# Optimization experiments

Measured on AMD Instinct MI355X. Metric: run time of the kernel, lower is better.

## Reference

```python
import jax, jax.numpy as jnp
import numpy as np

N, C, T, H, W = 256, 512, 4, 8, 8
NUM_CLIPS = 8


def conv3(x, w):
    # x: [N,C,T,H,W], w: [O,I,1,3,3], padding (0,1,1) as in HR2O_NL
    return jax.lax.conv_general_dilated(
        x, w, window_strides=(1, 1, 1),
        padding=((0, 0), (1, 1), (1, 1)),
        dimension_numbers=('NCDHW', 'OIDHW', 'NCDHW'))


def setup_inputs() -> dict:
    key = jax.random.key(0)
    ks = jax.random.split(key, 8)
    w_scale = 1.0 / np.sqrt(C * 9)
    return {
        'x': jax.random.normal(ks[0], (N, C, T, H, W), dtype=jnp.float32),
        'roi_inds': jax.random.randint(ks[1], (N,), 0, NUM_CLIPS, dtype=jnp.int32),
        'Wq': jax.random.normal(ks[2], (C, C, 1, 3, 3), dtype=jnp.float32) * w_scale,
        'Wk': jax.random.normal(ks[3], (C, C, 1, 3, 3), dtype=jnp.float32) * w_scale,
        'Wv': jax.random.normal(ks[4], (C, C, 1, 3, 3), dtype=jnp.float32) * w_scale,
        'Wc': jax.random.normal(ks[5], (C, C, 1, 3, 3), dtype=jnp.float32) * w_scale,
        'gn_gamma': jnp.ones((C,), dtype=jnp.float32),
        'gn_beta': jnp.zeros((C,), dtype=jnp.float32),
    }


def reference(x, roi_inds, Wq, Wk, Wv, Wc, gn_gamma, gn_beta):
    q = conv3(x, Wq)            # [N,C,T,H,W]
    k = conv3(x, Wk)
    v = conv3(x, Wv)
    scale = 1.0 / jnp.sqrt(jnp.asarray(C, x.dtype))
    # pairwise channel dot per spatiotemporal location: [N,N,T,H,W]
    att = jnp.einsum('icthw,jcthw->ijthw', q, k) * scale
    same_group = (roi_inds[:, None] == roi_inds[None, :])  # [N,N]
    att = jnp.where(same_group[:, :, None, None, None], att, -jnp.inf)
    att = jax.nn.softmax(att, axis=1)  # per-group softmax (diagonal always valid)
    virt = jnp.einsum('ijthw,jcthw->icthw', att, v)  # [N,C,T,H,W]
    # GroupNorm, num_groups=1 (normalize over C,T,H,W per sample), affine
    mu = virt.mean(axis=(1, 2, 3, 4), keepdims=True)
    var = virt.var(axis=(1, 2, 3, 4), keepdims=True)
    virt = (virt - mu) * jax.lax.rsqrt(var + 1e-5)
    virt = virt * gn_gamma[None, :, None, None, None] + gn_beta[None, :, None, None, None]
    virt = jax.nn.relu(virt)
    virt = conv3(virt, Wc)
    return x + virt
```

## Files before the change

### kernel.cpp

```cpp
#include <hip/hip_runtime.h>
#include <hip/hip_bf16.h>

#define NN 256
#define CCH 512
#define TT 4
#define SS 64
#define LL 256

typedef unsigned short u16;
typedef unsigned int u32;

typedef __bf16 bf16_t;
typedef bf16_t bf16x8 __attribute__((ext_vector_type(8)));
typedef float f32x16 __attribute__((ext_vector_type(16)));

__device__ __forceinline__ float bf2f(u32 h){
    return __uint_as_float(h << 16);
}
__device__ __forceinline__ u16 f2bf(float f){
    u32 u = __float_as_uint(f);
    u32 r = u + 0x7fffu + ((u >> 16) & 1u);
    return (u16)(r >> 16);
}
__device__ __forceinline__ bf16x8 ldg8(const u16* p){
    uint4 q = *(const uint4*)p;
    return __builtin_bit_cast(bf16x8, q);
}
__device__ __forceinline__ bf16x8 ldl8(const u16* p){
    uint2 a = *(const uint2*)p;
    uint2 b = *(const uint2*)(p + 4);
    uint4 q; q.x = a.x; q.y = a.y; q.z = b.x; q.w = b.y;
    return __builtin_bit_cast(bf16x8, q);
}

__global__ __launch_bounds__(256) void wt_kernel(
    const float* __restrict__ W, u16* __restrict__ Wt)
{
    const int e = blockIdx.x * 256 + threadIdx.x;
    const int cl  = e & 15;
    const int o   = (e >> 4) & 511;
    const int cg  = (e >> 13) & 31;
    const int tap = e >> 18;
    Wt[e] = f2bf(W[((size_t)o * CCH + cg * 16 + cl) * 9 + tap]);
}

__global__ __launch_bounds__(256, 2) void conv_mfma_kernel(
    const float* __restrict__ x, const u16* __restrict__ Wt, u16* __restrict__ outb)
{
    __shared__ u16 lds[4 * 100 * 36];
    const int tid = threadIdx.x;
    const int n  = blockIdx.x;
    const int ob = blockIdx.y * 128;
    const int lane = tid & 63;
    const int w  = tid >> 6;
    const int wm = w & 1, wn = w >> 1;
    const int h   = lane >> 5;
    const int col = lane & 31;
    const int r  = col >> 3, cc = col & 7;

    for (int i = tid; i < 7200; i += 256) ((u32*)lds)[i] = 0;

    f32x16 acc[2][4];
    #pragma unroll
    for (int m = 0; m < 2; ++m)
      #pragma unroll
      for (int j = 0; j < 4; ++j)
        #pragma unroll
        for (int e = 0; e < 16; ++e) acc[m][j][e] = 0.f;

    const int cp2 = tid >> 4;
    const int s4  = (tid & 15) << 2;

    int bbase[4];
    #pragma unroll
    for (int j = 0; j < 4; ++j){
        const int nt = wn * 4 + j;
        const int p = nt >> 1, sh = nt & 1;
        bbase[j] = (p * 100 + (sh * 4 + r) * 10 + cc) * 36 + h * 8;
    }
    const size_t abase = (size_t)(ob + wm * 64 + col) * 16 + h * 8;

    for (int ch = 0; ch < 16; ++ch){
        const int c0 = ch * 32;
        __syncthreads();
        #pragma unroll
        for (int p = 0; p < 4; ++p){
            const float* xr = x + (((size_t)n * CCH + c0 + 2 * cp2) * TT + p) * SS + s4;
            const float4 v0 = *(const float4*)xr;
            const float4 v1 = *(const float4*)(xr + 256);
            const float a0[4] = {v0.x, v0.y, v0.z, v0.w};
            const float a1[4] = {v1.x, v1.y, v1.z, v1.w};
            #pragma unroll
            for (int i = 0; i < 4; ++i){
                const int s = s4 + i;
                const int sp = ((s >> 3) + 1) * 10 + (s & 7) + 1;
                ((u32*)lds)[(p * 100 + sp) * 18 + cp2] =
                    (u32)f2bf(a0[i]) | ((u32)f2bf(a1[i]) << 16);
            }
        }
        __syncthreads();
        #pragma unroll
        for (int tap = 0; tap < 9; ++tap){
            const int tof = ((tap / 3) * 10 + (tap % 3)) * 36;
            #pragma unroll
            for (int ks = 0; ks < 2; ++ks){
                const size_t ai = (size_t)(tap * 32 + ch * 2 + ks) * 8192 + abase;
                const bf16x8 a0 = ldg8(Wt + ai);
                const bf16x8 a1 = ldg8(Wt + ai + 512);
                bf16x8 bfr[4];
                #pragma unroll
                for (int j = 0; j < 4; ++j)
                    bfr[j] = ldl8(&lds[bbase[j] + tof + ks * 16]);
                #pragma unroll
                for (int j = 0; j < 4; ++j){
                    acc[0][j] = __builtin_amdgcn_mfma_f32_32x32x16_bf16(a0, bfr[j], acc[0][j], 0, 0, 0);
                    acc[1][j] = __builtin_amdgcn_mfma_f32_32x32x16_bf16(a1, bfr[j], acc[1][j], 0, 0, 0);
                }
            }
        }
    }

    #pragma unroll
    for (int m = 0; m < 2; ++m){
        #pragma unroll
        for (int j = 0; j < 4; ++j){
            const int nt = wn * 4 + j;
            const int p = nt >> 1, sh = nt & 1;
            const int loc = p * SS + sh * 32 + col;
            u16* orow = outb + ((size_t)loc * NN + n) * CCH + ob + wm * 64 + m * 32;
            #pragma unroll
            for (int g2 = 0; g2 < 4; ++g2){
                uint2 val;
                val.x = (u32)f2bf(acc[m][j][g2 * 4 + 0]) | ((u32)f2bf(acc[m][j][g2 * 4 + 1]) << 16);
                val.y = (u32)f2bf(acc[m][j][g2 * 4 + 2]) | ((u32)f2bf(acc[m][j][g2 * 4 + 3]) << 16);
                *(uint2*)&orow[g2 * 8 + h * 4] = val;
            }
        }
    }
}

__global__ __launch_bounds__(256, 2) void conv_out_mfma_kernel(
    const u16* __restrict__ virtb, const u16* __restrict__ Wt,
    const float* __restrict__ x, const float* __restrict__ gamma,
    const float* __restrict__ beta, const float* __restrict__ musig,
    float* __restrict__ out)
{
    __shared__ u16 lds[4 * 100 * 36];
    const int tid = threadIdx.x;
    const int n  = blockIdx.x;
    const int ob = blockIdx.y * 128;
    const int lane = tid & 63;
    const int w  = tid >> 6;
    const int wm = w & 1, wn = w >> 1;
    const int h   = lane >> 5;
    const int col = lane & 31;
    const int r  = col >> 3, cc = col & 7;

    const float mu   = musig[2 * n];
    const float rsig = musig[2 * n + 1];

    for (int i = tid; i < 7200; i += 256) ((u32*)lds)[i] = 0;

    f32x16 acc[2][4];
    #pragma unroll
    for (int m = 0; m < 2; ++m)
      #pragma unroll
      for (int j = 0; j < 4; ++j)
        #pragma unroll
        for (int e = 0; e < 16; ++e) acc[m][j][e] = 0.f;

    const int cp = tid & 15;
    const int sg = tid >> 4;

    int bbase[4];
    #pragma unroll
    for (int j = 0; j < 4; ++j){
        const int nt = wn * 4 + j;
        const int p = nt >> 1, sh = nt & 1;
        bbase[j] = (p * 100 + (sh * 4 + r) * 10 + cc) * 36 + h * 8;
    }
    const size_t abase = (size_t)(ob + wm * 64 + col) * 16 + h * 8;

    for (int ch = 0; ch < 16; ++ch){
        const int c0 = ch * 32;
        const float g0 = gamma[c0 + 2 * cp], g1 = gamma[c0 + 2 * cp + 1];
        const float b0 = beta [c0 + 2 * cp], b1 = beta [c0 + 2 * cp + 1];
        __syncthreads();
        #pragma unroll
        for (int p = 0; p < 4; ++p){
            #pragma unroll
            for (int i = 0; i < 4; ++i){
                const int s = sg * 4 + i;
                const u32 wv = *(const u32*)(virtb + ((size_t)(p * SS + s) * NN + n) * CCH + c0 + 2 * cp);
                const float f0 = fmaxf((bf2f(wv & 0xffffu) - mu) * rsig * g0 + b0, 0.f);
                const float f1 = fmaxf((bf2f(wv >> 16)     - mu) * rsig * g1 + b1, 0.f);
                const int sp = ((s >> 3) + 1) * 10 + (s & 7) + 1;
                ((u32*)lds)[(p * 100 + sp) * 18 + cp] =
                    (u32)f2bf(f0) | ((u32)f2bf(f1) << 16);
            }
        }
        __syncthreads();
        #pragma unroll
        for (int tap = 0; tap < 9; ++tap){
            const int tof = ((tap / 3) * 10 + (tap % 3)) * 36;
            #pragma unroll
            for (int ks = 0; ks < 2; ++ks){
                const size_t ai = (size_t)(tap * 32 + ch * 2 + ks) * 8192 + abase;
                const bf16x8 a0 = ldg8(Wt + ai);
                const bf16x8 a1 = ldg8(Wt + ai + 512);
                bf16x8 bfr[4];
                #pragma unroll
                for (int j = 0; j < 4; ++j)
                    bfr[j] = ldl8(&lds[bbase[j] + tof + ks * 16]);
                #pragma unroll
                for (int j = 0; j < 4; ++j){
                    acc[0][j] = __builtin_amdgcn_mfma_f32_32x32x16_bf16(a0, bfr[j], acc[0][j], 0, 0, 0);
                    acc[1][j] = __builtin_amdgcn_mfma_f32_32x32x16_bf16(a1, bfr[j], acc[1][j], 0, 0, 0);
                }
            }
        }
    }

    #pragma unroll
    for (int m = 0; m < 2; ++m){
        #pragma unroll
        for (int j = 0; j < 4; ++j){
            const int nt = wn * 4 + j;
            const int p = nt >> 1, sh = nt & 1;
            const int s = sh * 32 + col;
            #pragma unroll
            for (int g2 = 0; g2 < 4; ++g2){
                const int o0 = ob + wm * 64 + m * 32 + 8 * g2 + 4 * h;
                #pragma unroll
                for (int rr = 0; rr < 4; ++rr){
                    const size_t oi = (((size_t)n * CCH + o0 + rr) * TT + p) * SS + s;
                    out[oi] = x[oi] + acc[m][j][g2 * 4 + rr];
                }
            }
        }
    }
}

__global__ __launch_bounds__(256) void vt_kernel(
    const u16* __restrict__ vb, u16* __restrict__ vt)
{
    __shared__ u16 ts[64][72];
    const int loc = blockIdx.x;
    const int n0 = (blockIdx.y & 3) * 64;
    const int c0 = (blockIdx.y >> 2) * 64;
    const int tid = threadIdx.x;
    const int rr = tid >> 3;
    const int ct = tid & 7;
    #pragma unroll
    for (int q = 0; q < 2; ++q){
        const int row = rr + q * 32;
        const int key = (row & 7) ^ ((row >> 3) & 7);
        const uint4 v = *(const uint4*)(vb + ((size_t)loc * NN + n0 + row) * CCH + c0 + ct * 8);
        *(uint4*)&ts[row][(ct ^ key) << 3] = v;
    }
    __syncthreads();
    #pragma unroll
    for (int q = 0; q < 2; ++q){
        const int c = rr + q * 32;
        u16 tmp[8];
        #pragma unroll
        for (int e = 0; e < 8; ++e){
            const int n = ct * 8 + e;
            const int key = (n & 7) ^ ((n >> 3) & 7);
            tmp[e] = ts[n][(((c >> 3) ^ key) << 3) + (c & 7)];
        }
        uint4 o;
        o.x = (u32)tmp[0] | ((u32)tmp[1] << 16);
        o.y = (u32)tmp[2] | ((u32)tmp[3] << 16);
        o.z = (u32)tmp[4] | ((u32)tmp[5] << 16);
        o.w = (u32)tmp[6] | ((u32)tmp[7] << 16);
        *(uint4*)(vt + ((size_t)loc * CCH + c0 + c) * NN + n0 + ct * 8) = o;
    }
}

__global__ __launch_bounds__(256, 3) void attn_mfma_kernel(
    const u16* __restrict__ qb, const u16* __restrict__ kb,
    const u16* __restrict__ vt, const int* __restrict__ roi,
    u16* __restrict__ virtb)
{
    __shared__ float Srow[32][264];
    __shared__ u16 Pfrag[16 * 64 * 8];
    __shared__ int roi_s[256];

    const int bid = blockIdx.x;
    const int loc = ((bid >> 6) << 3) | (bid & 7);
    const int it  = (bid >> 3) & 7;
    const int i0  = it * 32;
    const int tid = threadIdx.x;
    const int lane = tid & 63;
    const int w   = tid >> 6;
    const int h   = lane >> 5;
    const int col = lane & 31;

    roi_s[tid] = roi[tid];

    f32x16 acc0, acc1;
    #pragma unroll
    for (int e = 0; e < 16; ++e){ acc0[e] = 0.f; acc1[e] = 0.f; }

    const u16* qp = qb + ((size_t)loc * NN + i0 + col) * CCH + h * 8;
    const u16* kp = kb + ((size_t)loc * NN + w * 64 + col) * CCH + h * 8;

    #pragma unroll 4
    for (int kc = 0; kc < 32; ++kc){
        const bf16x8 a  = ldg8(qp + kc * 16);
        const bf16x8 b0 = ldg8(kp + kc * 16);
        const bf16x8 b1 = ldg8(kp + 32 * CCH + kc * 16);
        acc0 = __builtin_amdgcn_mfma_f32_32x32x16_bf16(a, b0, acc0, 0, 0, 0);
        acc1 = __builtin_amdgcn_mfma_f32_32x32x16_bf16(a, b1, acc1, 0, 0, 0);
    }

    #pragma unroll
    for (int e = 0; e < 16; ++e){
        const int r = (e & 3) + 8 * (e >> 2) + 4 * h;
        Srow[r][w * 64 + col]      = acc0[e];
        Srow[r][w * 64 + 32 + col] = acc1[e];
    }
    __syncthreads();

    {
        const int row = tid >> 3, u = tid & 7;
        const int myroi = roi_s[i0 + row];
        const float scale = 0.04419417382415922f;
        float ev[32];
        float mx = -1e30f;
        #pragma unroll
        for (int g = 0; g < 8; ++g){
            const float4 s4 = *(const float4*)&Srow[row][u * 4 + g * 32];
            const float ss[4] = {s4.x, s4.y, s4.z, s4.w};
            #pragma unroll
            for (int q = 0; q < 4; ++q){
                const int j = u * 4 + g * 32 + q;
                const float xv = (roi_s[j] == myroi) ? ss[q] * scale : -1e30f;
                ev[g * 4 + q] = xv;
                mx = fmaxf(mx, xv);
            }
        }
        mx = fmaxf(mx, __shfl_xor(mx, 1));
        mx = fmaxf(mx, __shfl_xor(mx, 2));
        mx = fmaxf(mx, __shfl_xor(mx, 4));
        float ssum = 0.f;
        #pragma unroll
        for (int q2 = 0; q2 < 32; ++q2){
            const float e2 = (ev[q2] > -1e29f) ? __expf(ev[q2] - mx) : 0.f;
            ev[q2] = e2;
            ssum += e2;
        }
// ... 27 lines not shown
        #pragma unroll
        for (int jn = 0; jn < 4; ++jn){
            const bf16x8 bv = ldg8(vp + (size_t)(jn * 32) * NN + t * 16);
            pacc[jn] = __builtin_amdgcn_mfma_f32_32x32x16_bf16(pa, bv, pacc[jn], 0, 0, 0);
        }
    }

    u16* op = virtb + ((size_t)loc * NN + i0) * CCH + w * 128 + col;
    #pragma unroll
    for (int jn = 0; jn < 4; ++jn){
        #pragma unroll
        for (int e = 0; e < 16; ++e){
            const int r = (e & 3) + 8 * (e >> 2) + 4 * h;
            op[(size_t)r * CCH + jn * 32] = f2bf(pacc[jn][e]);
        }
    }
}

__global__ __launch_bounds__(256) void stats_kernel(
    const u16* __restrict__ virtb, float* __restrict__ musig)
{
    const int n = blockIdx.x;
    const int tid = threadIdx.x;
    float s = 0.f, q = 0.f;
    for (int loc = 0; loc < LL; ++loc){
        const u32 v = *(const u32*)(virtb + ((size_t)loc * NN + n) * CCH + 2 * tid);
        const float a = bf2f(v & 0xffffu);
        const float b = bf2f(v >> 16);
        s += a + b;
        q += a * a + b * b;
    }
    #pragma unroll
    for (int off = 1; off < 64; off <<= 1){
        s += __shfl_xor(s, off);
        q += __shfl_xor(q, off);
    }
    __shared__ float red[8];
    const int wave = tid >> 6;
    if ((tid & 63) == 0){ red[wave * 2] = s; red[wave * 2 + 1] = q; }
    __syncthreads();
    if (tid == 0){
        const float S = red[0] + red[2] + red[4] + red[6];
        const float Q = red[1] + red[3] + red[5] + red[7];
        const float inv = 1.f / 131072.f;
        const float mval = S * inv;
        const float var = Q * inv - mval * mval;
        musig[2 * n]     = mval;
        musig[2 * n + 1] = rsqrtf(var + 1e-5f);
    }
}

__global__ void sentinel_kernel(float* out){
    const size_t i = (size_t)blockIdx.x * 256 + threadIdx.x;
    out[i] = 1.0e9f;
}

extern "C" void kernel_launch(void* const* d_in, const int* in_sizes, int n_in,
                              void* d_out, int out_size, void* d_ws, size_t ws_size,
                              hipStream_t stream)
{
    (void)in_sizes; (void)n_in; (void)out_size;
    const float* x   = (const float*)d_in[0];
    const int*   roi = (const int*)d_in[1];
    const float* Wq  = (const float*)d_in[2];
    const float* Wk  = (const float*)d_in[3];
    const float* Wv  = (const float*)d_in[4];
    const float* Wc  = (const float*)d_in[5];
    const float* gam = (const float*)d_in[6];
    const float* bet = (const float*)d_in[7];
    float* out = (float*)d_out;

    const size_t EL = 33554432ull;
    const size_t need = EL * 2ull * 4ull + 2048ull;
    if (ws_size < need){
        sentinel_kernel<<<131072, 256, 0, stream>>>(out);
        return;
    }
    u16* qb    = (u16*)d_ws;
    u16* kb    = qb + EL;
    u16* vb    = kb + EL;
    u16* virtb = vb + EL;
    float* musig = (float*)(virtb + EL);

    u16* WtA = (u16*)d_out;
    u16* vt  = (u16*)d_out + (1u << 22);
    u16* WtC = qb;

    const dim3 cgrid(256, 4);

    wt_kernel<<<9216, 256, 0, stream>>>(Wq, WtA);
    conv_mfma_kernel<<<cgrid, 256, 0, stream>>>(x, WtA, qb);
    wt_kernel<<<9216, 256, 0, stream>>>(Wk, WtA);
    conv_mfma_kernel<<<cgrid, 256, 0, stream>>>(x, WtA, kb);
    wt_kernel<<<9216, 256, 0, stream>>>(Wv, WtA);
    conv_mfma_kernel<<<cgrid, 256, 0, stream>>>(x, WtA, vb);

    vt_kernel<<<dim3(256, 32), 256, 0, stream>>>(vb, vt);
    attn_mfma_kernel<<<2048, 256, 0, stream>>>(qb, kb, vt, roi, virtb);
    stats_kernel<<<256, 256, 0, stream>>>(virtb, musig);

    wt_kernel<<<9216, 256, 0, stream>>>(Wc, WtC);
    conv_out_mfma_kernel<<<cgrid, 256, 0, stream>>>(virtb, WtC, x, gam, bet, musig, out);
}
```

Before: 1.734 ms.

## Give each wave a private double-buffered LDS tile and drop block barriers in convs

Both conv kernels now give each wave ownership of one time slice (p = wave index) with its own double-buffered LDS region. That removes the block-wide __syncthreads, and the next channel chunk's global loads overlap the current chunk's MFMAs. Each wave now computes 128 output channels by 64 spatial positions (4x2 tiles) instead of 64x128, which changes the A/B operand reuse mix. The LDS row stride is padded from 36 to 40 so B fragments load as single 16-byte reads, and input staging uses 16-byte stores. The costs are more LDS per block (64KB), more global A-fragment loads per wave, and more registers held by the prefetch buffers, which may hurt occupancy.

```diff
diff --git a/kernel.cpp b/kernel.cpp
--- a/kernel.cpp
+++ b/kernel.cpp
@@ -24,12 +24,6 @@
 }
 __device__ __forceinline__ bf16x8 ldg8(const u16* p){
     uint4 q = *(const uint4*)p;
-    return __builtin_bit_cast(bf16x8, q);
-}
-__device__ __forceinline__ bf16x8 ldl8(const u16* p){
-    uint2 a = *(const uint2*)p;
-    uint2 b = *(const uint2*)(p + 4);
-    uint4 q; q.x = a.x; q.y = a.y; q.z = b.x; q.w = b.y;
     return __builtin_bit_cast(bf16x8, q);
 }
 
@@ -47,92 +41,105 @@
 __global__ __launch_bounds__(256, 2) void conv_mfma_kernel(
     const float* __restrict__ x, const u16* __restrict__ Wt, u16* __restrict__ outb)
 {
-    __shared__ u16 lds[4 * 100 * 36];
+    __shared__ u16 lds[8 * 4000];
     const int tid = threadIdx.x;
     const int n  = blockIdx.x;
     const int ob = blockIdx.y * 128;
     const int lane = tid & 63;
     const int w  = tid >> 6;
-    const int wm = w & 1, wn = w >> 1;
     const int h   = lane >> 5;
     const int col = lane & 31;
     const int r  = col >> 3, cc = col & 7;
 
-    for (int i = tid; i < 7200; i += 256) ((u32*)lds)[i] = 0;
-
-    f32x16 acc[2][4];
-    #pragma unroll
-    for (int m = 0; m < 2; ++m)
+    {
+        u32* wb = (u32*)(lds + w * 8000);
+        for (int i = lane; i < 4000; i += 64) wb[i] = 0;
+    }
+
+    f32x16 acc[4][2];
+    #pragma unroll
+    for (int m = 0; m < 4; ++m)
       #pragma unroll
-      for (int j = 0; j < 4; ++j)
-        #pragma unroll
-        for (int e = 0; e < 16; ++e) acc[m][j][e] = 0.f;
-
-    const int cp2 = tid >> 4;
-    const int s4  = (tid & 15) << 2;
-
-    int bbase[4];
-    #pragma unroll
-    for (int j = 0; j < 4; ++j){
-        const int nt = wn * 4 + j;
-        const int p = nt >> 1, sh = nt & 1;
-        bbase[j] = (p * 100 + (sh * 4 + r) * 10 + cc) * 36 + h * 8;
-    }
-    const size_t abase = (size_t)(ob + wm * 64 + col) * 16 + h * 8;
+      for (int nt = 0; nt < 2; ++nt)
+        #pragma unroll
+        for (int e = 0; e < 16; ++e) acc[m][nt][e] = 0.f;
+
+    const int g  = lane >> 4;
+    const int s4 = (lane & 15) << 2;
+
+    int bbase[2];
+    #pragma unroll
+    for (int nt = 0; nt < 2; ++nt)
+        bbase[nt] = ((nt * 4 + r) * 10 + cc) * 40 + h * 8;
+
+    const size_t abase = (size_t)(ob + col) * 16 + h * 8;
+
+    auto stage_load = [&](int ch, float4* xv){
+        const float* xr = x + (((size_t)n * CCH + ch * 32 + g * 8) * TT + w) * SS + s4;
+        #pragma unroll
+        for (int c2 = 0; c2 < 8; ++c2)
+            xv[c2] = *(const float4*)(xr + (size_t)c2 * (TT * SS));
+    };
+    auto stage_write = [&](int ch, const float4* xv){
+        u16* wb = lds + w * 8000 + (ch & 1) * 4000;
+        #pragma unroll
+        for (int i = 0; i < 4; ++i){
+            const int s = s4 + i;
+            const int sp = ((s >> 3) + 1) * 10 + (s & 7) + 1;
+            uint4 pw;
+            pw.x = (u32)f2bf(((const float*)&xv[0])[i]) | ((u32)f2bf(((const float*)&xv[1])[i]) << 16);
+            pw.y = (u32)f2bf(((const float*)&xv[2])[i]) | ((u32)f2bf(((const float*)&xv[3])[i]) << 16);
+            pw.z = (u32)f2bf(((const float*)&xv[4])[i]) | ((u32)f2bf(((const float*)&xv[5])[i]) << 16);
+            pw.w = (u32)f2bf(((const float*)&xv[6])[i]) | ((u32)f2bf(((const float*)&xv[7])[i]) << 16);
+            *(uint4*)&wb[sp * 40 + g * 8] = pw;
+        }
+    };
+
+    {
+        float4 xv[8];
+        stage_load(0, xv);
+        stage_write(0, xv);
+    }
 
     for (int ch = 0; ch < 16; ++ch){
-        const int c0 = ch * 32;
-        __syncthreads();
-        #pragma unroll
-        for (int p = 0; p < 4; ++p){
-            const float* xr = x + (((size_t)n * CCH + c0 + 2 * cp2) * TT + p) * SS + s4;
-            const float4 v0 = *(const float4*)xr;
-            const float4 v1 = *(const float4*)(xr + 256);
-            const float a0[4] = {v0.x, v0.y, v0.z, v0.w};
-            const float a1[4] = {v1.x, v1.y, v1.z, v1.w};
-            #pragma unroll
-            for (int i = 0; i < 4; ++i){
-                const int s = s4 + i;
-                const int sp = ((s >> 3) + 1) * 10 + (s & 7) + 1;
-                ((u32*)lds)[(p * 100 + sp) * 18 + cp2] =
-                    (u32)f2bf(a0[i]) | ((u32)f2bf(a1[i]) << 16);
-            }
-        }
-        __syncthreads();
+        float4 xv[8];
+        if (ch < 15) stage_load(ch + 1, xv);
+
+        const u16* wb = lds + w * 8000 + (ch & 1) * 4000;
         #pragma unroll
         for (int tap = 0; tap < 9; ++tap){
-            const int tof = ((tap / 3) * 10 + (tap % 3)) * 36;
+            const int tof = ((tap / 3) * 10 + (tap % 3)) * 40;
             #pragma unroll
             for (int ks = 0; ks < 2; ++ks){
                 const size_t ai = (size_t)(tap * 32 + ch * 2 + ks) * 8192 + abase;
-                const bf16x8 a0 = ldg8(Wt + ai);
-                const bf16x8 a1 = ldg8(Wt + ai + 512);
-                bf16x8 bfr[4];
-                #pragma unroll
-                for (int j = 0; j < 4; ++j)
-                    bfr[j] = ldl8(&lds[bbase[j] + tof + ks * 16]);
-                #pragma unroll
-                for (int j = 0; j < 4; ++j){
-                    acc[0][j] = __builtin_amdgcn_mfma_f32_32x32x16_bf16(a0, bfr[j], acc[0][j], 0, 0, 0);
-                    acc[1][j] = __builtin_amdgcn_mfma_f32_32x32x16_bf16(a1, bfr[j], acc[1][j], 0, 0, 0);
-                }
+                bf16x8 a[4];
+                #pragma unroll
+                for (int m = 0; m < 4; ++m) a[m] = ldg8(Wt + ai + 512 * m);
+                bf16x8 b[2];
+                #pragma unroll
+                for (int nt = 0; nt < 2; ++nt)
+                    b[nt] = ldg8(&wb[bbase[nt] + tof + ks * 16]);
+                #pragma unroll
+                for (int m = 0; m < 4; ++m)
+                  #pragma unroll
+                  for (int nt = 0; nt < 2; ++nt)
+                    acc[m][nt] = __builtin_amdgcn_mfma_f32_32x32x16_bf16(a[m], b[nt], acc[m][nt], 0, 0, 0);
             }
         }
-    }
-
-    #pragma unroll
-    for (int m = 0; m < 2; ++m){
-        #pragma unroll
-        for (int j = 0; j < 4; ++j){
-            const int nt = wn * 4 + j;
-            const int p = nt >> 1, sh = nt & 1;
-            const int loc = p * SS + sh * 32 + col;
-            u16* orow = outb + ((size_t)loc * NN + n) * CCH + ob + wm * 64 + m * 32;
+        if (ch < 15) stage_write(ch + 1, xv);
+    }
+
+    #pragma unroll
+    for (int m = 0; m < 4; ++m){
+        #pragma unroll
+        for (int nt = 0; nt < 2; ++nt){
+            const int loc = w * 64 + nt * 32 + col;
+            u16* orow = outb + ((size_t)loc * NN + n) * CCH + ob + m * 32;
             #pragma unroll
             for (int g2 = 0; g2 < 4; ++g2){
                 uint2 val;
-                val.x = (u32)f2bf(acc[m][j][g2 * 4 + 0]) | ((u32)f2bf(acc[m][j][g2 * 4 + 1]) << 16);
-                val.y = (u32)f2bf(acc[m][j][g2 * 4 + 2]) | ((u32)f2bf(acc[m][j][g2 * 4 + 3]) << 16);
+                val.x = (u32)f2bf(acc[m][nt][g2 * 4 + 0]) | ((u32)f2bf(acc[m][nt][g2 * 4 + 1]) << 16);
+                val.y = (u32)f2bf(acc[m][nt][g2 * 4 + 2]) | ((u32)f2bf(acc[m][nt][g2 * 4 + 3]) << 16);
                 *(uint2*)&orow[g2 * 8 + h * 4] = val;
             }
         }
@@ -145,13 +152,12 @@
     const float* __restrict__ beta, const float* __restrict__ musig,
     float* __restrict__ out)
 {
-    __shared__ u16 lds[4 * 100 * 36];
+    __shared__ u16 lds[8 * 4000];
     const int tid = threadIdx.x;
     const int n  = blockIdx.x;
     const int ob = blockIdx.y * 128;
     const int lane = tid & 63;
     const int w  = tid >> 6;
-    const int wm = w & 1, wn = w >> 1;
     const int h   = lane >> 5;
     const int col = lane & 31;
     const int r  = col >> 3, cc = col & 7;
@@ -159,82 +165,117 @@
     const float mu   = musig[2 * n];
     const float rsig = musig[2 * n + 1];
 
-    for (int i = tid; i < 7200; i += 256) ((u32*)lds)[i] = 0;
-
-    f32x16 acc[2][4];
-    #pragma unroll
-    for (int m = 0; m < 2; ++m)
+    {
+        u32* wb = (u32*)(lds + w * 8000);
+        for (int i = lane; i < 4000; i += 64) wb[i] = 0;
+    }
+
+    f32x16 acc[4][2];
+    #pragma unroll
+    for (int m = 0; m < 4; ++m)
       #pragma unroll
-      for (int j = 0; j < 4; ++j)
-        #pragma unroll
-        for (int e = 0; e < 16; ++e) acc[m][j][e] = 0.f;
-
-    const int cp = tid & 15;
-    const int sg = tid >> 4;
-
-    int bbase[4];
-    #pragma unroll
-    for (int j = 0; j < 4; ++j){
-        const int nt = wn * 4 + j;
-        const int p = nt >> 1, sh = nt & 1;
-        bbase[j] = (p * 100 + (sh * 4 + r) * 10 + cc) * 36 + h * 8;
-    }
-    const size_t abase = (size_t)(ob + wm * 64 + col) * 16 + h * 8;
+      for (int nt = 0; nt < 2; ++nt)
+        #pragma unroll
+        for (int e = 0; e < 16; ++e) acc[m][nt][e] = 0.f;
+
+    const int g  = lane >> 4;
+    const int s4 = (lane & 15) << 2;
+
+    int bbase[2];
+    #pragma unroll
+    for (int nt = 0; nt < 2; ++nt)
+        bbase[nt] = ((nt * 4 + r) * 10 + cc) * 40 + h * 8;
+
+    const size_t abase = (size_t)(ob + col) * 16 + h * 8;
+
+    auto stage_load = [&](int ch, uint4* vv){
+        #pragma unroll
+        for (int i = 0; i < 4; ++i)
+            vv[i] = *(const uint4*)(virtb + ((size_t)(w * 64 + s4 + i) * NN + n) * CCH + ch * 32 + g * 8);
+    };
+    auto stage_write = [&](int ch, const uint4* vv){
+        const float* gp = gamma + ch * 32 + g * 8;
+        const float* bp = beta  + ch * 32 + g * 8;
+        const float4 ga0 = *(const float4*)gp;
+        const float4 ga1 = *(const float4*)(gp + 4);
+        const float4 be0 = *(const float4*)bp;
+        const float4 be1 = *(const float4*)(bp + 4);
+        float gsc[8], off[8];
+        const float gav[8] = {ga0.x, ga0.y, ga0.z, ga0.w, ga1.x, ga1.y, ga1.z, ga1.w};
+        const float bev[8] = {be0.x, be0.y, be0.z, be0.w, be1.x, be1.y, be1.z, be1.w};
+        #pragma unroll
+        for (int c2 = 0; c2 < 8; ++c2){
+            gsc[c2] = gav[c2] * rsig;
+            off[c2] = bev[c2] - mu * rsig * gav[c2];
+        }
+        u16* wb = lds + w * 8000 + (ch & 1) * 4000;
+        #pragma unroll
+        for (int i = 0; i < 4; ++i){
+            const int s = s4 + i;
+            const int sp = ((s >> 3) + 1) * 10 + (s & 7) + 1;
+            const u32 q[4] = {vv[i].x, vv[i].y, vv[i].z, vv[i].w};
+            u16 ov[8];
+            #pragma unroll
+            for (int c2 = 0; c2 < 8; ++c2){
+                const u32 half = (c2 & 1) ? (q[c2 >> 1] >> 16) : (q[c2 >> 1] & 0xffffu);
+                const float f = fmaxf(bf2f(half) * gsc[c2] + off[c2], 0.f);
+                ov[c2] = f2bf(f);
+            }
+            uint4 pw;
+            pw.x = (u32)ov[0] | ((u32)ov[1] << 16);
+            pw.y = (u32)ov[2] | ((u32)ov[3] << 16);
+            pw.z = (u32)ov[4] | ((u32)ov[5] << 16);
+            pw.w = (u32)ov[6] | ((u32)ov[7] << 16);
+            *(uint4*)&wb[sp * 40 + g * 8] = pw;
+        }
+    };
+
+    {
+        uint4 vv[4];
+        stage_load(0, vv);
+        stage_write(0, vv);
+    }
 
     for (int ch = 0; ch < 16; ++ch){
-        const int c0 = ch * 32;
-        const float g0 = gamma[c0 + 2 * cp], g1 = gamma[c0 + 2 * cp + 1];
-        const float b0 = beta [c0 + 2 * cp], b1 = beta [c0 + 2 * cp + 1];
-        __syncthreads();
-        #pragma unroll
-        for (int p = 0; p < 4; ++p){
-            #pragma unroll
-            for (int i = 0; i < 4; ++i){
-                const int s = sg * 4 + i;
-                const u32 wv = *(const u32*)(virtb + ((size_t)(p * SS + s) * NN + n) * CCH + c0 + 2 * cp);
-                const float f0 = fmaxf((bf2f(wv & 0xffffu) - mu) * rsig * g0 + b0, 0.f);
-                const float f1 = fmaxf((bf2f(wv >> 16)     - mu) * rsig * g1 + b1, 0.f);
-                const int sp = ((s >> 3) + 1) * 10 + (s & 7) + 1;
-                ((u32*)lds)[(p * 100 + sp) * 18 + cp] =
-                    (u32)f2bf(f0) | ((u32)f2bf(f1) << 16);
-            }
-        }
-        __syncthreads();
+        uint4 vv[4];
+        if (ch < 15) stage_load(ch + 1, vv);
+
+        const u16* wb = lds + w * 8000 + (ch & 1) * 4000;
         #pragma unroll
         for (int tap = 0; tap < 9; ++tap){
-            const int tof = ((tap / 3) * 10 + (tap % 3)) * 36;
+            const int tof = ((tap / 3) * 10 + (tap % 3)) * 40;
             #pragma unroll
             for (int ks = 0; ks < 2; ++ks){
                 const size_t ai = (size_t)(tap * 32 + ch * 2 + ks) * 8192 + abase;
-                const bf16x8 a0 = ldg8(Wt + ai);
-                const bf16x8 a1 = ldg8(Wt + ai + 512);
-                bf16x8 bfr[4];
-                #pragma unroll
-                for (int j = 0; j < 4; ++j)
-                    bfr[j] = ldl8(&lds[bbase[j] + tof + ks * 16]);
-                #pragma unroll
-                for (int j = 0; j < 4; ++j){
-                    acc[0][j] = __builtin_amdgcn_mfma_f32_32x32x16_bf16(a0, bfr[j], acc[0][j], 0, 0, 0);
-                    acc[1][j] = __builtin_amdgcn_mfma_f32_32x32x16_bf16(a1, bfr[j], acc[1][j], 0, 0, 0);
-                }
+                bf16x8 a[4];
+                #pragma unroll
+                for (int m = 0; m < 4; ++m) a[m] = ldg8(Wt + ai + 512 * m);
+                bf16x8 b[2];
+                #pragma unroll
+                for (int nt = 0; nt < 2; ++nt)
+                    b[nt] = ldg8(&wb[bbase[nt] + tof + ks * 16]);
+                #pragma unroll
+                for (int m = 0; m < 4; ++m)
+                  #pragma unroll
+                  for (int nt = 0; nt < 2; ++nt)
+                    acc[m][nt] = __builtin_amdgcn_mfma_f32_32x32x16_bf16(a[m], b[nt], acc[m][nt], 0, 0, 0);
             }
         }
-    }
-
-    #pragma unroll
-    for (int m = 0; m < 2; ++m){
-        #pragma unroll
-        for (int j = 0; j < 4; ++j){
-            const int nt = wn * 4 + j;
-            const int p = nt >> 1, sh = nt & 1;
-            const int s = sh * 32 + col;
+        if (ch < 15) stage_write(ch + 1, vv);
+    }
+
+    #pragma unroll
+    for (int m = 0; m < 4; ++m){
+        #pragma unroll
+        for (int nt = 0; nt < 2; ++nt){
+            const int s = nt * 32 + col;
             #pragma unroll
             for (int g2 = 0; g2 < 4; ++g2){
-                const int o0 = ob + wm * 64 + m * 32 + 8 * g2 + 4 * h;
+                const int o0 = ob + m * 32 + 8 * g2 + 4 * h;
                 #pragma unroll
                 for (int rr = 0; rr < 4; ++rr){
-                    const size_t oi = (((size_t)n * CCH + o0 + rr) * TT + p) * SS + s;
-                    out[oi] = x[oi] + acc[m][j][g2 * 4 + rr];
+                    const size_t oi = (((size_t)n * CCH + o0 + rr) * TT + w) * SS + s;
+                    out[oi] = x[oi] + acc[m][nt][g2 * 4 + rr];
                 }
             }
         }
```

Result: slower. 2.108 ms (+21.5%).

## Double-buffer LDS input tiles and prefetch next channel chunk in both convs

Applied to the files above, without the earlier changes.

Both implicit-GEMM conv kernels now use two LDS buffers. The next 32-channel chunk is loaded from global memory into registers before the MFMA loop over the current chunk, then written into the other buffer afterwards, leaving one barrier per iteration instead of two. The LDS row stride goes from 36 to 40 halves so the B-fragment reads become single 16-byte loads, and the staging writes become 16-byte stores with a per-wave layout. In the output conv, the GroupNorm affine is folded into a scale and offset. The cost is LDS growing to about 64KB per block and extra registers for the prefetch, which could limit the two-blocks-per-CU occupancy.

```diff
diff --git a/kernel.cpp b/kernel.cpp
--- a/kernel.cpp
+++ b/kernel.cpp
@@ -24,12 +24,6 @@
 }
 __device__ __forceinline__ bf16x8 ldg8(const u16* p){
     uint4 q = *(const uint4*)p;
-    return __builtin_bit_cast(bf16x8, q);
-}
-__device__ __forceinline__ bf16x8 ldl8(const u16* p){
-    uint2 a = *(const uint2*)p;
-    uint2 b = *(const uint2*)(p + 4);
-    uint4 q; q.x = a.x; q.y = a.y; q.z = b.x; q.w = b.y;
     return __builtin_bit_cast(bf16x8, q);
 }
 
@@ -47,7 +41,7 @@
 __global__ __launch_bounds__(256, 2) void conv_mfma_kernel(
     const float* __restrict__ x, const u16* __restrict__ Wt, u16* __restrict__ outb)
 {
-    __shared__ u16 lds[4 * 100 * 36];
+    __shared__ u16 lds[2 * 4 * 100 * 40];
     const int tid = threadIdx.x;
     const int n  = blockIdx.x;
     const int ob = blockIdx.y * 128;
@@ -58,7 +52,7 @@
     const int col = lane & 31;
     const int r  = col >> 3, cc = col & 7;
 
-    for (int i = tid; i < 7200; i += 256) ((u32*)lds)[i] = 0;
+    for (int i = tid; i < 16000; i += 256) ((u32*)lds)[i] = 0;
 
     f32x16 acc[2][4];
     #pragma unroll
@@ -68,40 +62,55 @@
         #pragma unroll
         for (int e = 0; e < 16; ++e) acc[m][j][e] = 0.f;
 
-    const int cp2 = tid >> 4;
-    const int s4  = (tid & 15) << 2;
+    const int g  = lane >> 4;
+    const int sl = lane & 15;
 
     int bbase[4];
     #pragma unroll
     for (int j = 0; j < 4; ++j){
         const int nt = wn * 4 + j;
         const int p = nt >> 1, sh = nt & 1;
-        bbase[j] = (p * 100 + (sh * 4 + r) * 10 + cc) * 36 + h * 8;
+        bbase[j] = (p * 100 + (sh * 4 + r) * 10 + cc) * 40 + h * 8;
     }
     const size_t abase = (size_t)(ob + wm * 64 + col) * 16 + h * 8;
 
+    auto stage_load = [&](int ch, float4* xv){
+        const float* xr = x + (((size_t)n * CCH + ch * 32 + g * 8) * TT + w) * SS + sl * 4;
+        #pragma unroll
+        for (int c2 = 0; c2 < 8; ++c2)
+            xv[c2] = *(const float4*)(xr + (size_t)c2 * (TT * SS));
+    };
+    auto stage_write = [&](int buf, const float4* xv){
+        u16* wb = lds + buf * 16000 + w * 4000;
+        #pragma unroll
+        for (int i = 0; i < 4; ++i){
+            const int s = sl * 4 + i;
+            const int sp = ((s >> 3) + 1) * 10 + (s & 7) + 1;
+            uint4 pw;
+            pw.x = (u32)f2bf(((const float*)&xv[0])[i]) | ((u32)f2bf(((const float*)&xv[1])[i]) << 16);
+            pw.y = (u32)f2bf(((const float*)&xv[2])[i]) | ((u32)f2bf(((const float*)&xv[3])[i]) << 16);
+            pw.z = (u32)f2bf(((const float*)&xv[4])[i]) | ((u32)f2bf(((const float*)&xv[5])[i]) << 16);
+            pw.w = (u32)f2bf(((const float*)&xv[6])[i]) | ((u32)f2bf(((const float*)&xv[7])[i]) << 16);
+            *(uint4*)&wb[sp * 40 + g * 8] = pw;
+        }
+    };
+
+    {
+        float4 xv[8];
+        stage_load(0, xv);
+        __syncthreads();
+        stage_write(0, xv);
+    }
+    __syncthreads();
+
     for (int ch = 0; ch < 16; ++ch){
-        const int c0 = ch * 32;
-        __syncthreads();
-        #pragma unroll
-        for (int p = 0; p < 4; ++p){
-            const float* xr = x + (((size_t)n * CCH + c0 + 2 * cp2) * TT + p) * SS + s4;
-            const float4 v0 = *(const float4*)xr;
-            const float4 v1 = *(const float4*)(xr + 256);
-            const float a0[4] = {v0.x, v0.y, v0.z, v0.w};
-            const float a1[4] = {v1.x, v1.y, v1.z, v1.w};
-            #pragma unroll
-            for (int i = 0; i < 4; ++i){
-                const int s = s4 + i;
-                const int sp = ((s >> 3) + 1) * 10 + (s & 7) + 1;
-                ((u32*)lds)[(p * 100 + sp) * 18 + cp2] =
-                    (u32)f2bf(a0[i]) | ((u32)f2bf(a1[i]) << 16);
-            }
-        }
-        __syncthreads();
+        float4 xv[8];
+        if (ch < 15) stage_load(ch + 1, xv);
+
+        const u16* cb = lds + (ch & 1) * 16000;
         #pragma unroll
         for (int tap = 0; tap < 9; ++tap){
-            const int tof = ((tap / 3) * 10 + (tap % 3)) * 36;
+            const int tof = ((tap / 3) * 10 + (tap % 3)) * 40;
             #pragma unroll
             for (int ks = 0; ks < 2; ++ks){
                 const size_t ai = (size_t)(tap * 32 + ch * 2 + ks) * 8192 + abase;
@@ -110,7 +119,7 @@
                 bf16x8 bfr[4];
                 #pragma unroll
                 for (int j = 0; j < 4; ++j)
-                    bfr[j] = ldl8(&lds[bbase[j] + tof + ks * 16]);
+                    bfr[j] = ldg8(&cb[bbase[j] + tof + ks * 16]);
                 #pragma unroll
                 for (int j = 0; j < 4; ++j){
                     acc[0][j] = __builtin_amdgcn_mfma_f32_32x32x16_bf16(a0, bfr[j], acc[0][j], 0, 0, 0);
@@ -118,6 +127,8 @@
                 }
             }
         }
+        if (ch < 15) stage_write((ch + 1) & 1, xv);
+        __syncthreads();
     }
 
     #pragma unroll
@@ -145,7 +156,7 @@
     const float* __restrict__ beta, const float* __restrict__ musig,
     float* __restrict__ out)
 {
-    __shared__ u16 lds[4 * 100 * 36];
+    __shared__ u16 lds[2 * 4 * 100 * 40];
     const int tid = threadIdx.x;
     const int n  = blockIdx.x;
     const int ob = blockIdx.y * 128;
@@ -159,7 +170,7 @@
     const float mu   = musig[2 * n];
     const float rsig = musig[2 * n + 1];
 
-    for (int i = tid; i < 7200; i += 256) ((u32*)lds)[i] = 0;
+    for (int i = tid; i < 16000; i += 256) ((u32*)lds)[i] = 0;
 
     f32x16 acc[2][4];
     #pragma unroll
@@ -169,40 +180,78 @@
         #pragma unroll
         for (int e = 0; e < 16; ++e) acc[m][j][e] = 0.f;
 
-    const int cp = tid & 15;
-    const int sg = tid >> 4;
+    const int g  = lane >> 4;
+    const int sl = lane & 15;
 
     int bbase[4];
     #pragma unroll
     for (int j = 0; j < 4; ++j){
         const int nt = wn * 4 + j;
         const int p = nt >> 1, sh = nt & 1;
-        bbase[j] = (p * 100 + (sh * 4 + r) * 10 + cc) * 36 + h * 8;
+        bbase[j] = (p * 100 + (sh * 4 + r) * 10 + cc) * 40 + h * 8;
     }
     const size_t abase = (size_t)(ob + wm * 64 + col) * 16 + h * 8;
 
+    auto stage_load = [&](int ch, uint4* vv){
+        #pragma unroll
+        for (int i = 0; i < 4; ++i){
+            const int s = sl * 4 + i;
+            vv[i] = *(const uint4*)(virtb + ((size_t)(w * SS + s) * NN + n) * CCH + ch * 32 + g * 8);
+        }
+    };
+    auto stage_write = [&](int ch, int buf, const uint4* vv){
+        const float* gp = gamma + ch * 32 + g * 8;
+        const float* bp = beta  + ch * 32 + g * 8;
+        const float4 ga0 = *(const float4*)gp;
+        const float4 ga1 = *(const float4*)(gp + 4);
+        const float4 be0 = *(const float4*)bp;
+        const float4 be1 = *(const float4*)(bp + 4);
+        const float gav[8] = {ga0.x, ga0.y, ga0.z, ga0.w, ga1.x, ga1.y, ga1.z, ga1.w};
+        const float bev[8] = {be0.x, be0.y, be0.z, be0.w, be1.x, be1.y, be1.z, be1.w};
+        float gsc[8], off[8];
+        #pragma unroll
+        for (int c2 = 0; c2 < 8; ++c2){
+            gsc[c2] = gav[c2] * rsig;
+            off[c2] = bev[c2] - mu * rsig * gav[c2];
+        }
+        u16* wb = lds + buf * 16000 + w * 4000;
+        #pragma unroll
+        for (int i = 0; i < 4; ++i){
+            const int s = sl * 4 + i;
+            const int sp = ((s >> 3) + 1) * 10 + (s & 7) + 1;
+            const u32 q[4] = {vv[i].x, vv[i].y, vv[i].z, vv[i].w};
+            u16 ov[8];
+            #pragma unroll
+            for (int c2 = 0; c2 < 8; ++c2){
+                const u32 half = (c2 & 1) ? (q[c2 >> 1] >> 16) : (q[c2 >> 1] & 0xffffu);
+                const float f = fmaxf(bf2f(half) * gsc[c2] + off[c2], 0.f);
+                ov[c2] = f2bf(f);
+            }
+            uint4 pw;
+            pw.x = (u32)ov[0] | ((u32)ov[1] << 16);
+            pw.y = (u32)ov[2] | ((u32)ov[3] << 16);
+            pw.z = (u32)ov[4] | ((u32)ov[5] << 16);
+            pw.w = (u32)ov[6] | ((u32)ov[7] << 16);
+            *(uint4*)&wb[sp * 40 + g * 8] = pw;
+        }
+    };
+
+    {
+        uint4 vv[4];
+        stage_load(0, vv);
+        __syncthreads();
+        stage_write(0, 0, vv);
+    }
+    __syncthreads();
+
     for (int ch = 0; ch < 16; ++ch){
-        const int c0 = ch * 32;
-        const float g0 = gamma[c0 + 2 * cp], g1 = gamma[c0 + 2 * cp + 1];
-        const float b0 = beta [c0 + 2 * cp], b1 = beta [c0 + 2 * cp + 1];
-        __syncthreads();
-        #pragma unroll
-        for (int p = 0; p < 4; ++p){
-            #pragma unroll
-            for (int i = 0; i < 4; ++i){
-                const int s = sg * 4 + i;
-                const u32 wv = *(const u32*)(virtb + ((size_t)(p * SS + s) * NN + n) * CCH + c0 + 2 * cp);
-                const float f0 = fmaxf((bf2f(wv & 0xffffu) - mu) * rsig * g0 + b0, 0.f);
-                const float f1 = fmaxf((bf2f(wv >> 16)     - mu) * rsig * g1 + b1, 0.f);
-                const int sp = ((s >> 3) + 1) * 10 + (s & 7) + 1;
-                ((u32*)lds)[(p * 100 + sp) * 18 + cp] =
-                    (u32)f2bf(f0) | ((u32)f2bf(f1) << 16);
-            }
-        }
-        __syncthreads();
+        uint4 vv[4];
+        if (ch < 15) stage_load(ch + 1, vv);
+
+        const u16* cb = lds + (ch & 1) * 16000;
         #pragma unroll
         for (int tap = 0; tap < 9; ++tap){
-            const int tof = ((tap / 3) * 10 + (tap % 3)) * 36;
+            const int tof = ((tap / 3) * 10 + (tap % 3)) * 40;
             #pragma unroll
             for (int ks = 0; ks < 2; ++ks){
                 const size_t ai = (size_t)(tap * 32 + ch * 2 + ks) * 8192 + abase;
@@ -211,7 +260,7 @@
                 bf16x8 bfr[4];
                 #pragma unroll
                 for (int j = 0; j < 4; ++j)
-                    bfr[j] = ldl8(&lds[bbase[j] + tof + ks * 16]);
+                    bfr[j] = ldg8(&cb[bbase[j] + tof + ks * 16]);
                 #pragma unroll
                 for (int j = 0; j < 4; ++j){
                     acc[0][j] = __builtin_amdgcn_mfma_f32_32x32x16_bf16(a0, bfr[j], acc[0][j], 0, 0, 0);
@@ -219,6 +268,8 @@
                 }
             }
         }
+        if (ch < 15) stage_write(ch + 1, (ch + 1) & 1, vv);
+        __syncthreads();
     }
 
     #pragma unroll
```

Result: faster. 1.697 ms (-2.1%).

## Pre-pad bf16 conv inputs and double-buffer them into LDS via direct global-to-LDS loads

Applied to the files above, without the earlier changes.

Adds separate kernels that convert x, and the normalized virt (GroupNorm+ReLU folded in), into padded, XOR-swizzled bf16 tiles in global memory. The conv kernels then stream each 32-channel chunk straight into LDS with global_load_lds, double-buffered so the next chunk loads during the current MFMA work, and read 16-byte swizzled fragments from LDS. This removes per-block f32-to-bf16 conversion, LDS zeroing and one barrier per chunk. The block index is also remapped over a 1D grid. It costs two extra passes over memory and workspace reuse (xpad shares space with vt, virtn uses kb), which depends on the kernel ordering staying correct.

```diff
diff --git a/kernel.cpp b/kernel.cpp
--- a/kernel.cpp
+++ b/kernel.cpp
@@ -26,11 +26,10 @@
     uint4 q = *(const uint4*)p;
     return __builtin_bit_cast(bf16x8, q);
 }
-__device__ __forceinline__ bf16x8 ldl8(const u16* p){
-    uint2 a = *(const uint2*)p;
-    uint2 b = *(const uint2*)(p + 4);
-    uint4 q; q.x = a.x; q.y = a.y; q.z = b.x; q.w = b.y;
-    return __builtin_bit_cast(bf16x8, q);
+__device__ __forceinline__ void gload_lds16(const u16* g, u16* l){
+    __builtin_amdgcn_global_load_lds(
+        (const __attribute__((address_space(1))) void*)g,
+        (__attribute__((address_space(3))) void*)l, 16, 0, 0);
 }
 
 __global__ __launch_bounds__(256) void wt_kernel(
@@ -44,13 +43,121 @@
     Wt[e] = f2bf(W[((size_t)o * CCH + cg * 16 + cl) * 9 + tap]);
 }
 
+__global__ __launch_bounds__(256) void xpad_kernel(
+    const float* __restrict__ x, u16* __restrict__ xpad)
+{
+    const int n  = blockIdx.x;
+    const int ch = blockIdx.y;
+    const int tid = threadIdx.x;
+    const int p  = tid >> 6;
+    const int cb = (tid >> 4) & 3;
+    const int s4 = (tid & 15) << 2;
+    u16* tile = xpad + ((size_t)n * 16 + ch) * 12800;
+
+    const float* xr = x + (((size_t)n * CCH + ch * 32 + cb * 8) * TT + p) * SS + s4;
+    float4 v[8];
+    #pragma unroll
+    for (int c2 = 0; c2 < 8; ++c2)
+        v[c2] = *(const float4*)(xr + (size_t)c2 * (TT * SS));
+    #pragma unroll
+    for (int i = 0; i < 4; ++i){
+        const int s = s4 + i;
+        const int sp = ((s >> 3) + 1) * 10 + (s & 7) + 1;
+        const int q = cb ^ (sp & 3);
+        uint4 pw;
+        pw.x = (u32)f2bf(((const float*)&v[0])[i]) | ((u32)f2bf(((const float*)&v[1])[i]) << 16);
+        pw.y = (u32)f2bf(((const float*)&v[2])[i]) | ((u32)f2bf(((const float*)&v[3])[i]) << 16);
+        pw.z = (u32)f2bf(((const float*)&v[4])[i]) | ((u32)f2bf(((const float*)&v[5])[i]) << 16);
+        pw.w = (u32)f2bf(((const float*)&v[6])[i]) | ((u32)f2bf(((const float*)&v[7])[i]) << 16);
+        *(uint4*)&tile[p * 3200 + sp * 32 + q * 8] = pw;
+    }
+    for (int bt = tid; bt < 576; bt += 256){
+        const int pp   = bt / 144;
+        const int bb   = bt % 144;
+        const int bi   = bb >> 2;
+        const int slot = bb & 3;
+        int sp;
+        if (bi < 10)      sp = bi;
+        else if (bi < 20) sp = 90 + (bi - 10);
+        else { const int k = (bi - 20) >> 1; sp = (k + 1) * 10 + ((bi - 20) & 1) * 9; }
+        uint4 z; z.x = 0; z.y = 0; z.z = 0; z.w = 0;
+        *(uint4*)&tile[pp * 3200 + sp * 32 + slot * 8] = z;
+    }
+}
+
+__global__ __launch_bounds__(256) void virtn_kernel(
+    const u16* __restrict__ virtb, const float* __restrict__ musig,
+    const float* __restrict__ gamma, const float* __restrict__ beta,
+    u16* __restrict__ vn)
+{
+    const int n  = blockIdx.x;
+    const int ch = blockIdx.y;
+    const int tid = threadIdx.x;
+    const int p  = tid >> 6;
+    const int cb = (tid >> 4) & 3;
+    const int s4 = (tid & 15) << 2;
+    u16* tile = vn + ((size_t)n * 16 + ch) * 12800;
+
+    const float mu   = musig[2 * n];
+    const float rsig = musig[2 * n + 1];
+    const int c0 = ch * 32 + cb * 8;
+    const float4 ga0 = *(const float4*)(gamma + c0);
+    const float4 ga1 = *(const float4*)(gamma + c0 + 4);
+    const float4 be0 = *(const float4*)(beta + c0);
+    const float4 be1 = *(const float4*)(beta + c0 + 4);
+    const float gav[8] = {ga0.x, ga0.y, ga0.z, ga0.w, ga1.x, ga1.y, ga1.z, ga1.w};
+    const float bev[8] = {be0.x, be0.y, be0.z, be0.w, be1.x, be1.y, be1.z, be1.w};
+    float gsc[8], off[8];
+    #pragma unroll
+    for (int c2 = 0; c2 < 8; ++c2){
+        gsc[c2] = gav[c2] * rsig;
+        off[c2] = bev[c2] - mu * rsig * gav[c2];
+    }
+
+    #pragma unroll
+    for (int i = 0; i < 4; ++i){
+        const int s = s4 + i;
+        const int loc = p * SS + s;
+        const uint4 wv = *(const uint4*)(virtb + ((size_t)loc * NN + n) * CCH + c0);
+        const u32 q4[4] = {wv.x, wv.y, wv.z, wv.w};
+        u16 ov[8];
+        #pragma unroll
+        for (int c2 = 0; c2 < 8; ++c2){
+            const u32 half = (c2 & 1) ? (q4[c2 >> 1] >> 16) : (q4[c2 >> 1] & 0xffffu);
+            ov[c2] = f2bf(fmaxf(bf2f(half) * gsc[c2] + off[c2], 0.f));
+        }
+        const int sp = ((s >> 3) + 1) * 10 + (s & 7) + 1;
+        const int q = cb ^ (sp & 3);
+        uint4 pw;
+        pw.x = (u32)ov[0] | ((u32)ov[1] << 16);
+        pw.y = (u32)ov[2] | ((u32)ov[3] << 16);
+        pw.z = (u32)ov[4] | ((u32)ov[5] << 16);
+        pw.w = (u32)ov[6] | ((u32)ov[7] << 16);
+        *(uint4*)&tile[p * 3200 + sp * 32 + q * 8] = pw;
+    }
+    for (int bt = tid; bt < 576; bt += 256){
+        const int pp   = bt / 144;
+        const int bb   = bt % 144;
+        const int bi   = bb >> 2;
+        const int slot = bb & 3;
+        int sp;
+        if (bi < 10)      sp = bi;
+        else if (bi < 20) sp = 90 + (bi - 10);
+        else { const int k = (bi - 20) >> 1; sp = (k + 1) * 10 + ((bi - 20) & 1) * 9; }
+        uint4 z; z.x = 0; z.y = 0; z.z = 0; z.w = 0;
+        *(uint4*)&tile[pp * 3200 + sp * 32 + slot * 8] = z;
+    }
+}
+
 __global__ __launch_bounds__(256, 2) void conv_mfma_kernel(
-    const float* __restrict__ x, const u16* __restrict__ Wt, u16* __restrict__ outb)
-{
-    __shared__ u16 lds[4 * 100 * 36];
-    const int tid = threadIdx.x;
-    const int n  = blockIdx.x;
-    const int ob = blockIdx.y * 128;
+    const u16* __restrict__ xp, const u16* __restrict__ Wt, u16* __restrict__ outb)
+{
+    __shared__ u16 lds[2 * 12800];
+    const int bid = blockIdx.x;
+    const int wk  = (bid & 7) * 128 + (bid >> 3);
+    const int n  = wk >> 2;
+    const int ob = (wk & 3) * 128;
+    const int tid = threadIdx.x;
     const int lane = tid & 63;
     const int w  = tid >> 6;
     const int wm = w & 1, wn = w >> 1;
@@ -58,8 +165,6 @@
     const int col = lane & 31;
     const int r  = col >> 3, cc = col & 7;
 
-    for (int i = tid; i < 7200; i += 256) ((u32*)lds)[i] = 0;
-
     f32x16 acc[2][4];
     #pragma unroll
     for (int m = 0; m < 2; ++m)
@@ -68,40 +173,31 @@
         #pragma unroll
         for (int e = 0; e < 16; ++e) acc[m][j][e] = 0.f;
 
-    const int cp2 = tid >> 4;
-    const int s4  = (tid & 15) << 2;
-
-    int bbase[4];
+    int pb[4], sp0[4];
     #pragma unroll
     for (int j = 0; j < 4; ++j){
         const int nt = wn * 4 + j;
-        const int p = nt >> 1, sh = nt & 1;
-        bbase[j] = (p * 100 + (sh * 4 + r) * 10 + cc) * 36 + h * 8;
+        pb[j]  = (nt >> 1) * 3200;
+        sp0[j] = ((nt & 1) * 4 + r) * 10 + cc;
     }
     const size_t abase = (size_t)(ob + wm * 64 + col) * 16 + h * 8;
+    const u16* srcn = xp + (size_t)n * (16 * 12800) + lane * 8;
+
+    auto stage = [&](int ch, int buf){
+        const u16* g = srcn + (size_t)ch * 12800;
+        for (int i = w; i < 25; i += 4)
+            gload_lds16(g + i * 512, &lds[buf * 12800 + i * 512]);
+    };
+
+    stage(0, 0);
+    __syncthreads();
 
     for (int ch = 0; ch < 16; ++ch){
-        const int c0 = ch * 32;
-        __syncthreads();
-        #pragma unroll
-        for (int p = 0; p < 4; ++p){
-            const float* xr = x + (((size_t)n * CCH + c0 + 2 * cp2) * TT + p) * SS + s4;
-            const float4 v0 = *(const float4*)xr;
-            const float4 v1 = *(const float4*)(xr + 256);
-            const float a0[4] = {v0.x, v0.y, v0.z, v0.w};
-            const float a1[4] = {v1.x, v1.y, v1.z, v1.w};
-            #pragma unroll
-            for (int i = 0; i < 4; ++i){
-                const int s = s4 + i;
-                const int sp = ((s >> 3) + 1) * 10 + (s & 7) + 1;
-                ((u32*)lds)[(p * 100 + sp) * 18 + cp2] =
-                    (u32)f2bf(a0[i]) | ((u32)f2bf(a1[i]) << 16);
-            }
-        }
-        __syncthreads();
+        if (ch < 15) stage(ch + 1, (ch + 1) & 1);
+        const u16* cbuf = &lds[(ch & 1) * 12800];
         #pragma unroll
         for (int tap = 0; tap < 9; ++tap){
-            const int tof = ((tap / 3) * 10 + (tap % 3)) * 36;
+            const int T = (tap / 3) * 10 + (tap % 3);
             #pragma unroll
             for (int ks = 0; ks < 2; ++ks){
                 const size_t ai = (size_t)(tap * 32 + ch * 2 + ks) * 8192 + abase;
@@ -109,8 +205,11 @@
                 const bf16x8 a1 = ldg8(Wt + ai + 512);
                 bf16x8 bfr[4];
                 #pragma unroll
-                for (int j = 0; j < 4; ++j)
-                    bfr[j] = ldl8(&lds[bbase[j] + tof + ks * 16]);
+                for (int j = 0; j < 4; ++j){
+                    const int sp = sp0[j] + T;
+                    const int idx = pb[j] + sp * 32 + ((((ks << 1) | h) ^ (sp & 3)) << 3);
+                    bfr[j] = ldg8(&cbuf[idx]);
+                }
                 #pragma unroll
                 for (int j = 0; j < 4; ++j){
                     acc[0][j] = __builtin_amdgcn_mfma_f32_32x32x16_bf16(a0, bfr[j], acc[0][j], 0, 0, 0);
@@ -118,6 +217,7 @@
                 }
             }
         }
+        __syncthreads();
     }
 
     #pragma unroll
@@ -140,15 +240,15 @@
 }
 
 __global__ __launch_bounds__(256, 2) void conv_out_mfma_kernel(
-    const u16* __restrict__ virtb, const u16* __restrict__ Wt,
-    const float* __restrict__ x, const float* __restrict__ gamma,
-    const float* __restrict__ beta, const float* __restrict__ musig,
-    float* __restrict__ out)
-{
-    __shared__ u16 lds[4 * 100 * 36];
-    const int tid = threadIdx.x;
-    const int n  = blockIdx.x;
-    const int ob = blockIdx.y * 128;
+    const u16* __restrict__ vnp, const u16* __restrict__ Wt,
+    const float* __restrict__ x, float* __restrict__ out)
+{
+    __shared__ u16 lds[2 * 12800];
+    const int bid = blockIdx.x;
+    const int wk  = (bid & 7) * 128 + (bid >> 3);
+    const int n  = wk >> 2;
+    const int ob = (wk & 3) * 128;
+    const int tid = threadIdx.x;
     const int lane = tid & 63;
     const int w  = tid >> 6;
     const int wm = w & 1, wn = w >> 1;
@@ -156,11 +256,6 @@
     const int col = lane & 31;
     const int r  = col >> 3, cc = col & 7;
 
-    const float mu   = musig[2 * n];
-    const float rsig = musig[2 * n + 1];
-
-    for (int i = tid; i < 7200; i += 256) ((u32*)lds)[i] = 0;
-
     f32x16 acc[2][4];
     #pragma unroll
     for (int m = 0; m < 2; ++m)
@@ -169,40 +264,31 @@
         #pragma unroll
         for (int e = 0; e < 16; ++e) acc[m][j][e] = 0.f;
 
-    const int cp = tid & 15;
-    const int sg = tid >> 4;
-
-    int bbase[4];
+    int pb[4], sp0[4];
     #pragma unroll
     for (int j = 0; j < 4; ++j){
         const int nt = wn * 4 + j;
-        const int p = nt >> 1, sh = nt & 1;
-        bbase[j] = (p * 100 + (sh * 4 + r) * 10 + cc) * 36 + h * 8;
+        pb[j]  = (nt >> 1) * 3200;
+        sp0[j] = ((nt & 1) * 4 + r) * 10 + cc;
     }
     const size_t abase = (size_t)(ob + wm * 64 + col) * 16 + h * 8;
+    const u16* srcn = vnp + (size_t)n * (16 * 12800) + lane * 8;
+
+    auto stage = [&](int ch, int buf){
+        const u16* g = srcn + (size_t)ch * 12800;
+        for (int i = w; i < 25; i += 4)
+            gload_lds16(g + i * 512, &lds[buf * 12800 + i * 512]);
+    };
+
+    stage(0, 0);
+    __syncthreads();
 
     for (int ch = 0; ch < 16; ++ch){
-        const int c0 = ch * 32;
-        const float g0 = gamma[c0 + 2 * cp], g1 = gamma[c0 + 2 * cp + 1];
-        const float b0 = beta [c0 + 2 * cp], b1 = beta [c0 + 2 * cp + 1];
-        __syncthreads();
-        #pragma unroll
-        for (int p = 0; p < 4; ++p){
-            #pragma unroll
-            for (int i = 0; i < 4; ++i){
-                const int s = sg * 4 + i;
-                const u32 wv = *(const u32*)(virtb + ((size_t)(p * SS + s) * NN + n) * CCH + c0 + 2 * cp);
-                const float f0 = fmaxf((bf2f(wv & 0xffffu) - mu) * rsig * g0 + b0, 0.f);
-                const float f1 = fmaxf((bf2f(wv >> 16)     - mu) * rsig * g1 + b1, 0.f);
-                const int sp = ((s >> 3) + 1) * 10 + (s & 7) + 1;
-                ((u32*)lds)[(p * 100 + sp) * 18 + cp] =
-                    (u32)f2bf(f0) | ((u32)f2bf(f1) << 16);
-            }
-        }
-        __syncthreads();
+        if (ch < 15) stage(ch + 1, (ch + 1) & 1);
+        const u16* cbuf = &lds[(ch & 1) * 12800];
         #pragma unroll
         for (int tap = 0; tap < 9; ++tap){
-            const int tof = ((tap / 3) * 10 + (tap % 3)) * 36;
+            const int T = (tap / 3) * 10 + (tap % 3);
             #pragma unroll
             for (int ks = 0; ks < 2; ++ks){
                 const size_t ai = (size_t)(tap * 32 + ch * 2 + ks) * 8192 + abase;
@@ -210,8 +296,11 @@
                 const bf16x8 a1 = ldg8(Wt + ai + 512);
                 bf16x8 bfr[4];
                 #pragma unroll
-                for (int j = 0; j < 4; ++j)
-                    bfr[j] = ldl8(&lds[bbase[j] + tof + ks * 16]);
+                for (int j = 0; j < 4; ++j){
+                    const int sp = sp0[j] + T;
+                    const int idx = pb[j] + sp * 32 + ((((ks << 1) | h) ^ (sp & 3)) << 3);
+                    bfr[j] = ldg8(&cbuf[idx]);
+                }
                 #pragma unroll
                 for (int j = 0; j < 4; ++j){
                     acc[0][j] = __builtin_amdgcn_mfma_f32_32x32x16_bf16(a0, bfr[j], acc[0][j], 0, 0, 0);
@@ -219,6 +308,7 @@
                 }
             }
         }
+        __syncthreads();
     }
 
     #pragma unroll
@@ -265,9 +355,9 @@
         u16 tmp[8];
         #pragma unroll
         for (int e = 0; e < 8; ++e){
-            const int n = ct * 8 + e;
-            const int key = (n & 7) ^ ((n >> 3) & 7);
-            tmp[e] = ts[n][(((c >> 3) ^ key) << 3) + (c & 7)];
+            const int nn = ct * 8 + e;
+            const int key = (nn & 7) ^ ((nn >> 3) & 7);
+            tmp[e] = ts[nn][(((c >> 3) ^ key) << 3) + (c & 7)];
         }
         uint4 o;
         o.x = (u32)tmp[0] | ((u32)tmp[1] << 16);
@@ -461,23 +551,26 @@
     u16* virtb = vb + EL;
     float* musig = (float*)(virtb + EL);
 
-    u16* WtA = (u16*)d_out;
-    u16* vt  = (u16*)d_out + (1u << 22);
-    u16* WtC = qb;
-
-    const dim3 cgrid(256, 4);
+    u16* WtA  = (u16*)d_out;
+    u16* xpad = (u16*)d_out + (4u << 20);
+    u16* vt   = (u16*)d_out + (4u << 20);
+    u16* virtn = kb;
+    u16* WtC  = qb;
+
+    xpad_kernel<<<dim3(256, 16), 256, 0, stream>>>(x, xpad);
 
     wt_kernel<<<9216, 256, 0, stream>>>(Wq, WtA);
-    conv_mfma_kernel<<<cgrid, 256, 0, stream>>>(x, WtA, qb);
+    conv_mfma_kernel<<<1024, 256, 0, stream>>>(xpad, WtA, qb);
     wt_kernel<<<9216, 256, 0, stream>>>(Wk, WtA);
-    conv_mfma_kernel<<<cgrid, 256, 0, stream>>>(x, WtA, kb);
+    conv_mfma_kernel<<<1024, 256, 0, stream>>>(xpad, WtA, kb);
     wt_kernel<<<9216, 256, 0, stream>>>(Wv, WtA);
-    conv_mfma_kernel<<<cgrid, 256, 0, stream>>>(x, WtA, vb);
+    conv_mfma_kernel<<<1024, 256, 0, stream>>>(xpad, WtA, vb);
 
     vt_kernel<<<dim3(256, 32), 256, 0, stream>>>(vb, vt);
     attn_mfma_kernel<<<2048, 256, 0, stream>>>(qb, kb, vt, roi, virtb);
     stats_kernel<<<256, 256, 0, stream>>>(virtb, musig);
 
+    virtn_kernel<<<dim3(256, 16), 256, 0, stream>>>(virtb, musig, gam, bet, virtn);
     wt_kernel<<<9216, 256, 0, stream>>>(Wc, WtC);
-    conv_out_mfma_kernel<<<cgrid, 256, 0, stream>>>(virtb, WtC, x, gam, bet, musig, out);
-}
+    conv_out_mfma_kernel<<<1024, 256, 0, stream>>>(virtn, WtC, x, out);
+}
```

Result: faster. 1.595 ms (-8.0%).
